# Performance work log

Measured on AMD Instinct MI355X. Metric: run time of the kernel, lower is better.

The kernel has to match this reference:

```python
import jax, jax.numpy as jnp
import numpy as np

L, D, H, N, B2 = 9, 256, 4, 1024, 4   # layers, embed dim, heads, keypoints, 2*pairs
HD = D // H
THR = 0.1
MAXM = 50


def _linear(x, W, b):
    return x @ W.T + b


def _ln(x, g, b, eps=1e-5):
    m = jnp.mean(x, -1, keepdims=True)
    v = jnp.var(x, -1, keepdims=True)
    return (x - m) * jax.lax.rsqrt(v + eps) * g + b


def _ffn(x, w1, b1, g, bb, w2, b2):
    h = _linear(x, w1, b1)
    h = jax.nn.gelu(_ln(h, g, bb), approximate=False)
    return _linear(h, w2, b2)


def _mha(q, k, v):
    b, nq, _ = q.shape
    nk = k.shape[1]
    qh = q.reshape(b, nq, H, HD)
    kh = k.reshape(b, nk, H, HD)
    vh = v.reshape(b, nk, H, HD)
    s = jnp.einsum('bqhd,bkhd->bhqk', qh, kh) * (1.0 / np.float32(np.sqrt(HD)))
    a = jax.nn.softmax(s, -1)
    return jnp.einsum('bhqk,bkhd->bqhd', a, vh).reshape(b, nq, D)


def _rotate_half(qk):  # qk: [b, n, D, 2]
    b, n, _, _ = qk.shape
    r = qk.reshape(b, n, H, HD // 2, 2, 2)
    r = jnp.stack([-r[..., 1, :], r[..., 0, :]], axis=4)
    return r.reshape(b, n, D, 2)


def _posenc(kpts, Wr):
    proj = kpts @ Wr.T                    # [b, n, HD//2]
    def expand(t):
        t = jnp.repeat(t, 2, axis=-1)     # interleave -> [b, n, HD]
        return jnp.tile(t, (1, 1, H))     # -> [b, n, D]
    return jnp.stack([expand(jnp.cos(proj)), expand(jnp.sin(proj))])  # [2, b, n, D]


def _forward(kpts, desc, posenc_Wr,
             sWqkv_w, sWqkv_b, sOut_w, sOut_b, sF1_w, sF1_b, sLN_g, sLN_b, sF2_w, sF2_b,
             cQK_w, cQK_b, cV_w, cV_b, cOut_w, cOut_b, cF1_w, cF1_b, cLN_g, cLN_b, cF2_w, cF2_b,
             fp_w, fp_b, match_w, match_b):
    enc = _posenc(kpts, posenc_Wr)
    x = desc
    idx = np.arange(B2)
    swap = idx // 2 * 2 + (1 - idx % 2)   # swap images within each pair
    for i in range(L):
        # ---- self attention with cached rotary encoding ----
        b, n, _ = x.shape
        qkv = _linear(x, sWqkv_w[i], sWqkv_b[i]).reshape(b, n, D, 3)
        qk, v = qkv[..., :2], qkv[..., 2]
        qk = enc[0][..., None] * qk + enc[1][..., None] * _rotate_half(qk)
        ctx = _mha(qk[..., 0], qk[..., 1], v)
        msg = _linear(ctx, sOut_w[i], sOut_b[i])
        x = x + _ffn(jnp.concatenate([x, msg], -1),
                     sF1_w[i], sF1_b[i], sLN_g[i], sLN_b[i], sF2_w[i], sF2_b[i])
        # ---- cross attention between images of each pair ----
        qk = _linear(x, cQK_w[i], cQK_b[i])
        v = _linear(x, cV_w[i], cV_b[i])
        m = _mha(qk, qk[swap], v[swap])
        m = _linear(m, cOut_w[i], cOut_b[i])
        x = x + _ffn(jnp.concatenate([x, m], -1),
                     cF1_w[i], cF1_b[i], cLN_g[i], cLN_b[i], cF2_w[i], cF2_b[i])
    # ---- match assignment: sigmoid log double softmax ----
    md = _linear(x, fp_w, fp_b) / (D ** 0.25)
    sim = jnp.einsum('bnd,bmd->bnm', md[0::2], md[1::2])
    z = _linear(x, match_w, match_b)      # [B2, N, 1]
    cert = jax.nn.log_sigmoid(z[0::2]) + jnp.swapaxes(jax.nn.log_sigmoid(z[1::2]), 1, 2)
    return jax.nn.log_softmax(sim, 2) + jax.nn.log_softmax(sim, 1) + cert


def _filter_matches(scores):
    B = scores.shape[0]
    m0 = jnp.argmax(scores, 2)
    m1 = jnp.argmax(scores, 1)
    mscores = jnp.exp(jnp.max(scores, 2))
    mutual = jnp.arange(N)[None, :] == jnp.take_along_axis(m1, m0, 1)
    masked = mscores * ((mscores > THR) & mutual).astype(mscores.dtype)
    topk_scores, topk_idx = jax.lax.top_k(masked, MAXM)
    topk_m1 = jnp.take_along_axis(m0, topk_idx, 1)
    b_idx = jnp.broadcast_to(jnp.arange(B)[:, None], (B, MAXM))
    matches = jnp.stack([b_idx, topk_idx, topk_m1], 2)
    return matches[0], topk_scores[0]


def setup_inputs() -> dict:
    key = jax.random.key(0)
    ks = iter(jax.random.split(key, 48))
    def w(shape, scale=0.02):
        return jax.random.normal(next(ks), shape, jnp.float32) * scale
    inp = {
        'kpts': jax.random.normal(next(ks), (B2, N, 2), jnp.float32),
        'desc': jax.random.normal(next(ks), (B2, N, D), jnp.float32),
        'posenc_Wr': w((HD // 2, 2), 1.0),  # std = gamma**-2 = 1
        'sWqkv_w': w((L, 3 * D, D)), 'sWqkv_b': w((L, 3 * D)),
        'sOut_w': w((L, D, D)), 'sOut_b': w((L, D)),
        'sF1_w': w((L, 2 * D, 2 * D)), 'sF1_b': w((L, 2 * D)),
        'sLN_g': jnp.ones((L, 2 * D), jnp.float32), 'sLN_b': jnp.zeros((L, 2 * D), jnp.float32),
        'sF2_w': w((L, D, 2 * D)), 'sF2_b': w((L, D)),
        'cQK_w': w((L, D, D)), 'cQK_b': w((L, D)),
        'cV_w': w((L, D, D)), 'cV_b': w((L, D)),
        'cOut_w': w((L, D, D)), 'cOut_b': w((L, D)),
        'cF1_w': w((L, 2 * D, 2 * D)), 'cF1_b': w((L, 2 * D)),
        'cLN_g': jnp.ones((L, 2 * D), jnp.float32), 'cLN_b': jnp.zeros((L, 2 * D), jnp.float32),
        'cF2_w': w((L, D, 2 * D)), 'cF2_b': w((L, D)),
        'fp_w': w((D, D)), 'fp_b': w((D,)),
        'match_w': w((1, D)), 'match_b': w((1,)),
    }
    return inp


def reference(kpts, desc, posenc_Wr,
              sWqkv_w, sWqkv_b, sOut_w, sOut_b, sF1_w, sF1_b, sLN_g, sLN_b, sF2_w, sF2_b,
              cQK_w, cQK_b, cV_w, cV_b, cOut_w, cOut_b, cF1_w, cF1_b, cLN_g, cLN_b, cF2_w, cF2_b,
              fp_w, fp_b, match_w, match_b):
    scores = _forward(kpts, desc, posenc_Wr,
                      sWqkv_w, sWqkv_b, sOut_w, sOut_b, sF1_w, sF1_b, sLN_g, sLN_b, sF2_w, sF2_b,
                      cQK_w, cQK_b, cV_w, cV_b, cOut_w, cOut_b, cF1_w, cF1_b, cLN_g, cLN_b, cF2_w, cF2_b,
                      fp_w, fp_b, match_w, match_b)
    matches, mscores = _filter_matches(scores)
    return scores, matches, mscores
```

## Files before the change

### kernel.cpp

```cpp
#include <hip/hip_runtime.h>
#include <hip/hip_bf16.h>
#include <math.h>

typedef __hip_bfloat16 bf16;
typedef unsigned short ushort;
typedef unsigned int u32;
typedef __attribute__((ext_vector_type(8))) short s8b;
typedef __attribute__((ext_vector_type(4))) short s4b;
typedef __attribute__((ext_vector_type(4))) float f4v;

#define Nc 1024
#define Dc 256
#define MA 4096

__device__ __forceinline__ float tofl(float v){ return v; }
__device__ __forceinline__ float tofl(bf16 v){ return __bfloat162float(v); }

__device__ __forceinline__ ushort rneu(float f){
  unsigned u = __float_as_uint(f);
  unsigned r = (u + 0x7fffu + ((u>>16)&1u)) >> 16;
  return (ushort)r;
}
__device__ __forceinline__ float ubf(ushort h){ return __uint_as_float(((unsigned)h)<<16); }

__device__ __forceinline__ float fexp2(float x){
#if __has_builtin(__builtin_amdgcn_exp2f)
  return __builtin_amdgcn_exp2f(x);
#else
  return exp2f(x);
#endif
}

__global__ void k_detect(const void* p, int* flag){
  if(threadIdx.x==0 && blockIdx.x==0){
    *flag = (((const ushort*)p)[0] == 0x3F80) ? 0 : 1;
  }
}

template<typename TIN>
__device__ void gemm_body(const float* A, const TIN* B, const TIN* bias, float* C,
                          int M, int Nout, int K, int lda, int ldb, int ldc,
                          float alpha, int accum, int dolog){
  __shared__ float As[32][33];
  __shared__ float Bs[32][33];
  int tx = threadIdx.x, ty = threadIdx.y;
  int tid = ty*16 + tx;
  int n0 = blockIdx.x*32, m0 = blockIdx.y*32;
  int lr = tid >> 3;
  int lc = (tid & 7) * 4;
  float acc00=0.f, acc01=0.f, acc10=0.f, acc11=0.f;
  for(int kk=0; kk<K; kk+=32){
    int m = m0 + lr, n = n0 + lr;
#pragma unroll
    for(int j=0;j<4;j++){
      int k = kk + lc + j;
      As[lr][lc+j] = (m < M && k < K) ? A[(size_t)m*lda + k] : 0.f;
      Bs[lr][lc+j] = (n < Nout && k < K) ? tofl(B[(size_t)n*ldb + k]) : 0.f;
    }
    __syncthreads();
#pragma unroll
    for(int k=0;k<32;k++){
      float a0 = As[ty][k],   a1 = As[ty+16][k];
      float b0 = Bs[tx][k],   b1 = Bs[tx+16][k];
      acc00 += a0*b0; acc01 += a0*b1; acc10 += a1*b0; acc11 += a1*b1;
    }
    __syncthreads();
  }
#define STORE(mm,nn,acc) do{ int m_=(mm), n_=(nn); if(m_<M && n_<Nout){ \
    float r = (acc) + (bias ? tofl(bias[n_]) : 0.f); r *= alpha; \
    if(dolog) r = fminf(r,0.f) - log1pf(expf(-fabsf(r))); \
    if(accum) C[(size_t)m_*ldc + n_] += r; else C[(size_t)m_*ldc + n_] = r; } }while(0)
  STORE(m0+ty,    n0+tx,    acc00);
  STORE(m0+ty,    n0+tx+16, acc01);
  STORE(m0+ty+16, n0+tx,    acc10);
  STORE(m0+ty+16, n0+tx+16, acc11);
#undef STORE
}

__global__ __launch_bounds__(256)
void k_gemm_w(const int* flag, const float* A, const void* Bb, long boff,
              const void* biasb, long biasoff, float* C,
              int M, int Nout, int K, int lda, int ldb, int ldc,
              float alpha, int accum, int dolog){
  if(*flag){
    const float* B = ((const float*)Bb) + boff;
    const float* bi = biasb ? ((const float*)biasb) + biasoff : nullptr;
    gemm_body<float>(A, B, bi, C, M, Nout, K, lda, ldb, ldc, alpha, accum, dolog);
  }else{
    const bf16* B = ((const bf16*)Bb) + boff;
    const bf16* bi = biasb ? ((const bf16*)biasb) + biasoff : nullptr;
    gemm_body<bf16>(A, B, bi, C, M, Nout, K, lda, ldb, ldc, alpha, accum, dolog);
  }
}

template<typename TIN>
__device__ void cast2_body(const void* in_, float* x, ushort* xh, ushort* xl, int n){
  const TIN* in = (const TIN*)in_;
  int i = blockIdx.x*256 + threadIdx.x;
  if(i >= n) return;
  float f = tofl(in[i]);
  x[i] = f;
  ushort h = rneu(f);
  xh[i] = h; xl[i] = rneu(f - ubf(h));
}
__global__ void k_cast2(const int* flag, const void* in, float* x, ushort* xh, ushort* xl, int n){
  if(*flag) cast2_body<float>(in, x, xh, xl, n); else cast2_body<bf16>(in, x, xh, xl, n);
}

template<typename TIN>
__device__ void splitw_body(const void* src_, long off, ushort* dh, ushort* dl, int n){
  const TIN* src = ((const TIN*)src_) + off;
  int i = blockIdx.x*256 + threadIdx.x;
  if(i >= n) return;
  float f = tofl(src[i]);
  ushort h = rneu(f);
  dh[i] = h; dl[i] = rneu(f - ubf(h));
}
__global__ void k_splitw(const int* flag, const void* src, long off, ushort* dh, ushort* dl, int n){
  if(*flag) splitw_body<float>(src, off, dh, dl, n); else splitw_body<bf16>(src, off, dh, dl, n);
}
template<typename TIN>
__device__ void biasf_body(const void* src_, long off, float* dst, int n){
  const TIN* src = ((const TIN*)src_) + off;
  int i = blockIdx.x*256 + threadIdx.x;
  if(i < n) dst[i] = tofl(src[i]);
}
__global__ void k_biasf(const int* flag, const void* src, long off, float* dst, int n){
  if(*flag) biasf_body<float>(src, off, dst, n); else biasf_body<bf16>(src, off, dst, n);
}

template<typename TIN>
__device__ void rotcs_body(const void* kpts_, const void* Wr_, float* cs){
  int i = blockIdx.x*256 + threadIdx.x;
  if(i >= MA*32) return;
  int m = i >> 5, p = i & 31;
  const TIN* kpts = (const TIN*)kpts_;
  const TIN* Wr   = (const TIN*)Wr_;
  float kx = tofl(kpts[m*2]), ky = tofl(kpts[m*2+1]);
  float proj = kx*tofl(Wr[p*2]) + ky*tofl(Wr[p*2+1]);
  cs[(size_t)m*64 + p*2    ] = cosf(proj);
  cs[(size_t)m*64 + p*2 + 1] = sinf(proj);
}
__global__ void k_rotcs(const int* flag, const void* kpts, const void* Wr, float* cs){
  if(*flag) rotcs_body<float>(kpts, Wr, cs); else rotcs_body<bf16>(kpts, Wr, cs);
}

template<typename TIN>
__device__ void wsl_body(int L, const void* p0,const void* p1,const void* p2,const void* p3,
                         const void* p4,const void* p5,const void* p6,const void* p7,const void* p8,
                         const void* b0,const void* b1,const void* b2,const void* b3,const void* b4,
                         const void* b5,const void* b6,const void* b7,const void* b8,
                         ushort* WH, ushort* WL, float* WB){
  int idx = blockIdx.x*256 + threadIdx.x;
  if(idx < 311296){
    int i = idx*4;
    const TIN* s;
    if(i < 196608){
      int nr = i >> 8, col = i & 255;
      int sr = (nr < 256) ? nr*3 : (nr < 512) ? (nr-256)*3+1 : (nr-512)*3+2;
      s = (const TIN*)p0 + (size_t)L*196608 + sr*256 + col;
    }
    else if(i < 262144)  s = (const TIN*)p1 + (size_t)L*65536  + (i-196608);
    else if(i < 524288)  s = (const TIN*)p2 + (size_t)L*262144 + (i-262144);
    else if(i < 655360)  s = (const TIN*)p3 + (size_t)L*131072 + (i-524288);
    else if(i < 720896)  s = (const TIN*)p4 + (size_t)L*65536  + (i-655360);
    else if(i < 786432)  s = (const TIN*)p5 + (size_t)L*65536  + (i-720896);
    else if(i < 851968)  s = (const TIN*)p6 + (size_t)L*65536  + (i-786432);
    else if(i < 1114112) s = (const TIN*)p7 + (size_t)L*262144 + (i-851968);
    else                 s = (const TIN*)p8 + (size_t)L*131072 + (i-1114112);
    float f[4];
    if constexpr(sizeof(TIN) == 4){
      f4v v = *(const f4v*)s;
      f[0]=v[0]; f[1]=v[1]; f[2]=v[2]; f[3]=v[3];
    } else {
      s4b v = *(const s4b*)s;
#pragma unroll
      for(int j=0;j<4;j++) f[j] = __uint_as_float(((u32)(ushort)v[j])<<16);
    }
    s4b hv, lv;
#pragma unroll
    for(int j=0;j<4;j++){
      ushort h = rneu(f[j]);
      hv[j] = (short)h;
      lv[j] = (short)rneu(f[j] - ubf(h));
    }
    *(s4b*)&WH[i] = hv;
    *(s4b*)&WL[i] = lv;
  } else if(idx < 311296 + 3328){
    int j = idx - 311296;
    const TIN* s;
    if(j < 768){
      int sj = (j < 256) ? j*3 : (j < 512) ? (j-256)*3+1 : (j-512)*3+2;
      s = (const TIN*)b0 + (size_t)L*768 + sj;
    }
    else if(j < 1024)  s = (const TIN*)b1 + (size_t)L*256 + (j-768);
    else if(j < 1536)  s = (const TIN*)b2 + (size_t)L*512 + (j-1024);
    else if(j < 1792)  s = (const TIN*)b3 + (size_t)L*256 + (j-1536);
    else if(j < 2048)  s = (const TIN*)b4 + (size_t)L*256 + (j-1792);
    else if(j < 2304)  s = (const TIN*)b5 + (size_t)L*256 + (j-2048);
    else if(j < 2560)  s = (const TIN*)b6 + (size_t)L*256 + (j-2304);
    else if(j < 3072)  s = (const TIN*)b7 + (size_t)L*512 + (j-2560);
    else               s = (const TIN*)b8 + (size_t)L*256 + (j-3072);
    WB[j] = tofl(*s);
  }
}
__global__ void k_wsplit(const int* flag, int L0, long strW, long strB,
    const void* p0,const void* p1,const void* p2,const void* p3,const void* p4,
    const void* p5,const void* p6,const void* p7,const void* p8,
    const void* b0,const void* b1,const void* b2,const void* b3,const void* b4,
    const void* b5,const void* b6,const void* b7,const void* b8,
    ushort* WH, ushort* WL, float* WB){
  int L = L0 + blockIdx.y;
  ushort* WHl = WH + (size_t)blockIdx.y*strW;
  ushort* WLl = WL + (size_t)blockIdx.y*strW;
  float*  WBl = WB + (size_t)blockIdx.y*strB;
  if(*flag) wsl_body<float>(L,p0,p1,p2,p3,p4,p5,p6,p7,p8,b0,b1,b2,b3,b4,b5,b6,b7,b8,WHl,WLl,WBl);
  else      wsl_body<bf16>(L,p0,p1,p2,p3,p4,p5,p6,p7,p8,b0,b1,b2,b3,b4,b5,b6,b7,b8,WHl,WLl,WBl);
}

template<int MT>
__global__ __launch_bounds__(256)
void k_gemm_mxT(const ushort* __restrict__ Ah, const ushort* __restrict__ Al,
                const ushort* __restrict__ A2h, const ushort* __restrict__ A2l, int lda,
                const ushort* __restrict__ Bh, const ushort* __restrict__ Bl, int ldb,
                const float* __restrict__ bias, float alpha,
                float* C, int ldc, int accum,
                ushort* Ch, ushort* Cl, int lds,
                ushort* keh, ushort* kel, const float* __restrict__ cs,
                ushort* vth, ushort* vtl,
                int K, int mode){
  constexpr int MFR = MT/16;
  constexpr int NACC = MFR*2;
  constexpr int MFH = MFR/2;
  __shared__ __align__(16) ushort LB[(2*MT+128)*72];
  int t = threadIdx.x;
  int n0 = blockIdx.x*64, m0 = blockIdx.y*MT;
  int w = t>>6, lane = t&63, quad = lane>>4, l15 = lane&15;
  int kg = w>>1, nh = w&1;
  int brow = t>>2, bc16 = (t&3)*16;
  int arow = (MT==64) ? (t>>2) : (t>>3);
  int acol = (MT==64) ? ((t&3)*16) : ((t&7)*8);
  f4v acc[NACC];
  f4v zz = {0.f,0.f,0.f,0.f};
#pragma unroll
  for(int j=0;j<NACC;j++) acc[j] = zz;
  int rounds = K >> 6;

  s8b r0,r1,r2,r3,r4,r5,r6,r7;
  auto gload = [&](int r){
    int k0 = r*64;
    const ushort* ah = Ah; const ushort* al = Al; int kloc = k0;
    if(A2h && k0 >= 256){ ah = A2h; al = A2l; kloc = k0 - 256; }
    const ushort* aph = &ah[(size_t)(m0+arow)*lda + kloc + acol];
    const ushort* apl = &al[(size_t)(m0+arow)*lda + kloc + acol];
    const ushort* bph = &Bh[(size_t)(n0+brow)*ldb + k0 + bc16];
    const ushort* bpl = &Bl[(size_t)(n0+brow)*ldb + k0 + bc16];
    r0 = *(const s8b*)aph;
    r2 = *(const s8b*)apl;
    if(MT==64){ r1 = *(const s8b*)(aph+8); r3 = *(const s8b*)(apl+8); }
    r4 = *(const s8b*)bph;   r5 = *(const s8b*)(bph+8);
    r6 = *(const s8b*)bpl;   r7 = *(const s8b*)(bpl+8);
  };
  auto writeS = [&](){
    *(s8b*)&LB[(arow)*72 + acol]        = r0;
    *(s8b*)&LB[(MT+arow)*72 + acol]     = r2;
    if(MT==64){
      *(s8b*)&LB[(arow)*72 + acol+8]    = r1;
      *(s8b*)&LB[(MT+arow)*72 + acol+8] = r3;
    }
    *(s8b*)&LB[(2*MT+brow)*72 + bc16]      = r4;
    *(s8b*)&LB[(2*MT+brow)*72 + bc16+8]    = r5;
    *(s8b*)&LB[(2*MT+64+brow)*72 + bc16]   = r6;
    *(s8b*)&LB[(2*MT+64+brow)*72 + bc16+8] = r7;
  };

  gload(0);
  for(int r=0; r<rounds; r++){
    __syncthreads();
    writeS();
    __syncthreads();
    s8b afh[MFR], afl[MFR], bfh[2], bfl[2];
#pragma unroll
    for(int mf=0;mf<MFR;mf++){
      afh[mf] = *(s8b*)&LB[(mf*16+l15)*72 + kg*32+quad*8];
      afl[mf] = *(s8b*)&LB[(MT+mf*16+l15)*72 + kg*32+quad*8];
    }
#pragma unroll
    for(int nf=0;nf<2;nf++){
      bfh[nf] = *(s8b*)&LB[(2*MT+nh*32+nf*16+l15)*72 + kg*32+quad*8];
      bfl[nf] = *(s8b*)&LB[(2*MT+64+nh*32+nf*16+l15)*72 + kg*32+quad*8];
    }
    if(r+1 < rounds) gload(r+1);
#pragma unroll
    for(int mf=0;mf<MFR;mf++){
#pragma unroll
      for(int nf=0;nf<2;nf++){
        int a = mf*2+nf;
        acc[a] = __builtin_amdgcn_mfma_f32_16x16x32_bf16(afh[mf], bfh[nf], acc[a], 0,0,0);
        acc[a] = __builtin_amdgcn_mfma_f32_16x16x32_bf16(afh[mf], bfl[nf], acc[a], 0,0,0);
        acc[a] = __builtin_amdgcn_mfma_f32_16x16x32_bf16(afl[mf], bfh[nf], acc[a], 0,0,0);
      }
    }
  }
  __syncthreads();
  f4v* scr = (f4v*)LB;
#pragma unroll
  for(int f=0;f<NACC;f++) scr[(w*NACC+f)*64 + lane] = acc[f];
  __syncthreads();
  int pw = w^2;
#pragma unroll
  for(int f=0;f<NACC;f++){
    f4v o = scr[(pw*NACC+f)*64 + lane];
    acc[f] += o;
  }

  bool vblk = (mode == 1 && n0 >= 512) || (mode == 3 && n0 >= 256);
  if(vblk){
    __syncthreads();
    u32* tp = (u32*)LB;
#pragma unroll
    for(int mi=0;mi<MFH;mi++){
      int mf = kg*MFH + mi;
#pragma unroll
      for(int nf=0;nf<2;nf++){
        f4v a = acc[mf*2+nf];
#pragma unroll
        for(int rr=0;rr<4;rr++){
          int ml = mf*16 + quad*4 + rr;
          int nl = nh*32 + nf*16 + l15;
          float val = a[rr];
          if(bias) val += bias[n0 + nl];
          val *= alpha;
          ushort hh = rneu(val);
          ushort ll = rneu(val - ubf(hh));
          tp[nl*(MT+1) + ml] = (u32)hh | ((u32)ll << 16);
        }
      }
    }
    __syncthreads();
    int b = m0 >> 10;
    int mloc = m0 & 1023;
    int d0 = n0 - ((mode == 1) ? 512 : 256);
    constexpr int NPASS = (MT==64) ? 2 : 1;
#pragma unroll
    for(int pass=0; pass<NPASS; pass++){
      int row, col;
      if(MT==64){ row = (t>>3) + pass*32; col = (t&7)*8; }
      else      { row = t>>2;             col = (t&3)*8; }
      int d = d0 + row;
      u32 c0=tp[row*(MT+1)+col+0], c1=tp[row*(MT+1)+col+1], c2=tp[row*(MT+1)+col+2], c3=tp[row*(MT+1)+col+3];
      u32 c4=tp[row*(MT+1)+col+4], c5=tp[row*(MT+1)+col+5], c6=tp[row*(MT+1)+col+6], c7=tp[row*(MT+1)+col+7];
      s8b hi, lo;
      hi[0]=(short)(c0&0xffff); lo[0]=(short)(c0>>16);
      hi[1]=(short)(c1&0xffff); lo[1]=(short)(c1>>16);
      hi[2]=(short)(c2&0xffff); lo[2]=(short)(c2>>16);
      hi[3]=(short)(c3&0xffff); lo[3]=(short)(c3>>16);
      hi[4]=(short)(c4&0xffff); lo[4]=(short)(c4>>16);
      hi[5]=(short)(c5&0xffff); lo[5]=(short)(c5>>16);
      hi[6]=(short)(c6&0xffff); lo[6]=(short)(c6>>16);
      hi[7]=(short)(c7&0xffff); lo[7]=(short)(c7>>16);
      size_t go = ((size_t)((b*4 + (d>>6))*64 + (d&63)))*1024 + mloc + col;
      *(s8b*)&vth[go] = hi;
      *(s8b*)&vtl[go] = lo;
    }
    return;
  }

#pragma unroll
  for(int mi=0;mi<MFH;mi++){
    int mf = kg*MFH + mi;
#pragma unroll
    for(int nf=0;nf<2;nf++){
      f4v a = acc[mf*2+nf];
#pragma unroll
      for(int rr=0;rr<4;rr++){
        int m = m0 + mf*16 + quad*4 + rr;
        int n = n0 + nh*32 + nf*16 + l15;
        float val = a[rr];
        if(bias) val += bias[n];
        val *= alpha;
        if(mode == 1){
          int d = (n < 256) ? n : (n - 256);
          const float* csp = cs + (size_t)m*64 + (d & 62);
          float cc = csp[0], ssn = csp[1];
          float pv = __shfl_xor(val, 1);
          float rv = (d & 1) ? (cc*val + ssn*pv) : (cc*val - ssn*pv);
          ushort hh = rneu(rv);
          ushort* dh = (n < 256) ? Ch : keh;
          ushort* dl = (n < 256) ? Cl : kel;
          size_t gi = (size_t)m*256 + d;
          dh[gi] = hh; dl[gi] = rneu(rv - ubf(hh));
        } else if(mode == 3){
          ushort hh = rneu(val);
          Ch[(size_t)m*256 + n] = hh;
          Cl[(size_t)m*256 + n] = rneu(val - ubf(hh));
        } else {
          if(C){
            size_t ci = (size_t)m*ldc + n;
            if(accum) val += C[ci];
            C[ci] = val;
          }
          if(Ch){
            ushort hh = rneu(val);
            Ch[(size_t)m*lds + n] = hh;
            Cl[(size_t)m*lds + n] = rneu(val - ubf(hh));
          }
        }
      }
    }
  }
}

#define FSC 0.18033688011112042f
__global__ __launch_bounds__(256)
void k_flashmx(const ushort* __restrict__ qh_, const ushort* __restrict__ ql_,
               const ushort* __restrict__ kh_, const ushort* __restrict__ kl_,
               const ushort* __restrict__ vth_, const ushort* __restrict__ vtl_,
               ushort* __restrict__ cth, ushort* __restrict__ ctl, int bxor,
               float* __restrict__ PO, float* __restrict__ PML, int nch){
  int qt = blockIdx.x, z = blockIdx.y, ch = blockIdx.z;
  int b = z>>2, h = z&3;
  int bk = b ^ bxor;
  __shared__ __align__(16) ushort Kh[64][72], Kl[64][72], Vh[64][72], Vl[64][72];
  int t = threadIdx.x, w = t>>6, lane = t&63, quad = lane>>4, l15 = lane&15;
  ushort* Psw = &Kh[w*16][0];
  s8b qfh[2], qfl[2];
  {
    size_t row = (size_t)b*1024 + qt*64 + w*16 + l15;
    const ushort* qrh = qh_ + row*256 + h*64;
    const ushort* qrl = ql_ + row*256 + h*64;
    qfh[0] = *(const s8b*)(qrh + quad*8);
    qfh[1] = *(const s8b*)(qrh + 32 + quad*8);
    qfl[0] = *(const s8b*)(qrl + quad*8);
    qfl[1] = *(const s8b*)(qrl + 32 + quad*8);
  }
  float m_i[4] = {-1e30f,-1e30f,-1e30f,-1e30f};
  float l_i[4] = {0.f,0.f,0.f,0.f};
  f4v O[4];
  f4v zz = {0.f,0.f,0.f,0.f};
#pragma unroll
  for(int dt=0;dt<4;dt++) O[dt] = zz;

  s8b rK0,rK1,rK2,rK3, rV0,rV1,rV2,rV3;
  auto stage_load = [&](int kt){
#pragma unroll
    for(int i=0;i<4;i++){
      int c = t + i*256;
      int half = c>>9, row = (c>>3)&63, o8 = (c&7)*8;
      const s8b* src = (const s8b*)((half ? kl_ : kh_) +
                       ((size_t)(bk*1024 + kt*64 + row))*256 + h*64 + o8);
      if(i==0) rK0=*src; else if(i==1) rK1=*src; else if(i==2) rK2=*src; else rK3=*src;
    }
#pragma unroll
    for(int i=0;i<4;i++){
      int c = t + i*256;
      int half = c>>9, d = (c>>3)&63, o8 = (c&7)*8;
      const s8b* src = (const s8b*)((half ? vtl_ : vth_) +
                       ((size_t)((bk*4+h)*64 + d))*1024 + kt*64 + o8);
      if(i==0) rV0=*src; else if(i==1) rV1=*src; else if(i==2) rV2=*src; else rV3=*src;
    }
  };
  auto stage_write = [&](){
#pragma unroll
    for(int i=0;i<4;i++){
      int c = t + i*256;
      int half = c>>9, row = (c>>3)&63, o8 = (c&7)*8;
      s8b v = (i==0)?rK0:(i==1)?rK1:(i==2)?rK2:rK3;
      if(half) *(s8b*)&Kl[row][o8] = v;
      else     *(s8b*)&Kh[row][o8] = v;
    }
#pragma unroll
    for(int i=0;i<4;i++){
      int c = t + i*256;
      int half = c>>9, d = (c>>3)&63, o8 = (c&7)*8;
      s8b v = (i==0)?rV0:(i==1)?rV1:(i==2)?rV2:rV3;
      if(half) *(s8b*)&Vl[d][o8] = v;
      else     *(s8b*)&Vh[d][o8] = v;
    }
  };

  int ktn = 16/nch;
  int kt0 = ch*ktn;
  stage_load(kt0);
  for(int kt=kt0; kt<kt0+ktn; kt++){
    __syncthreads();
    stage_write();
    __syncthreads();
    if(kt+1 < kt0+ktn) stage_load(kt+1);
    f4v s[4];
#pragma unroll
    for(int nt=0;nt<4;nt++) s[nt] = zz;
#pragma unroll
    for(int nt=0;nt<4;nt++){
#pragma unroll
      for(int k2=0;k2<2;k2++){
        s8b fbh = *(s8b*)&Kh[nt*16+l15][k2*32 + quad*8];
        s8b fbl = *(s8b*)&Kl[nt*16+l15][k2*32 + quad*8];
        s[nt] = __builtin_amdgcn_mfma_f32_16x16x32_bf16(qfh[k2], fbh, s[nt], 0,0,0);
        s[nt] = __builtin_amdgcn_mfma_f32_16x16x32_bf16(qfh[k2], fbl, s[nt], 0,0,0);
        s[nt] = __builtin_amdgcn_mfma_f32_16x16x32_bf16(qfl[k2], fbh, s[nt], 0,0,0);
      }
    }
    __syncthreads();
#pragma unroll
    for(int rr=0;rr<4;rr++){
      float v0=s[0][rr]*FSC, v1=s[1][rr]*FSC, v2=s[2][rr]*FSC, v3=s[3][rr]*FSC;
      float mx = fmaxf(fmaxf(v0,v1), fmaxf(v2,v3));
      mx = fmaxf(mx, __shfl_xor(mx,1));
      mx = fmaxf(mx, __shfl_xor(mx,2));
      mx = fmaxf(mx, __shfl_xor(mx,4));
      mx = fmaxf(mx, __shfl_xor(mx,8));
      float mnew = fmaxf(m_i[rr], mx);
      float al = fexp2(m_i[rr] - mnew);
      float p0 = fexp2(v0-mnew), p1 = fexp2(v1-mnew), p2 = fexp2(v2-mnew), p3 = fexp2(v3-mnew);
      float ls = p0+p1+p2+p3;
      ls += __shfl_xor(ls,1);
      ls += __shfl_xor(ls,2);
      ls += __shfl_xor(ls,4);
      ls += __shfl_xor(ls,8);
      l_i[rr] = l_i[rr]*al + ls;
      m_i[rr] = mnew;
#pragma unroll
      for(int dt=0;dt<4;dt++) O[dt][rr] *= al;
      int prow = quad*4 + rr;
      Psw[prow*72 +  0 + l15] = rneu(p0);
      Psw[prow*72 + 16 + l15] = rneu(p1);
      Psw[prow*72 + 32 + l15] = rneu(p2);
      Psw[prow*72 + 48 + l15] = rneu(p3);
    }
    s8b pf0 = *(s8b*)&Psw[l15*72 + quad*8];
    s8b pf1 = *(s8b*)&Psw[l15*72 + 32 + quad*8];
#pragma unroll
    for(int dt=0;dt<4;dt++){
#pragma unroll
      for(int k2=0;k2<2;k2++){
        s8b fvh = *(s8b*)&Vh[dt*16+l15][k2*32 + quad*8];
        s8b fvl = *(s8b*)&Vl[dt*16+l15][k2*32 + quad*8];
        s8b pf = k2 ? pf1 : pf0;
        O[dt] = __builtin_amdgcn_mfma_f32_16x16x32_bf16(pf, fvh, O[dt], 0,0,0);
        O[dt] = __builtin_amdgcn_mfma_f32_16x16x32_bf16(pf, fvl, O[dt], 0,0,0);
      }
    }
  }
  if(nch == 1){
#pragma unroll
    for(int rr=0;rr<4;rr++){
      float inv = 1.f / l_i[rr];
      int row = qt*64 + w*16 + quad*4 + rr;
#pragma unroll
      for(int dt=0;dt<4;dt++){
        float val = O[dt][rr]*inv;
        size_t gi = ((size_t)b*1024 + row)*256 + h*64 + dt*16 + l15;
        ushort hh = rneu(val);
        cth[gi] = hh; ctl[gi] = rneu(val - ubf(hh));
      }
    }
  } else {
    size_t tb = (size_t)(z*16+qt)*nch + ch;
    float* po  = PO  + tb*4096;
    float* pml = PML + tb*128;
#pragma unroll
    for(int rr=0;rr<4;rr++){
      int row = w*16 + quad*4 + rr;
#pragma unroll
      for(int dt=0;dt<4;dt++){
        po[row*64 + dt*16 + l15] = O[dt][rr];
      }
      if(l15 == 0){
        pml[row]      = m_i[rr];
        pml[64 + row] = l_i[rr];
      }
    }
  }
}

__global__ __launch_bounds__(256)
void k_fmerge(const float* __restrict__ PO, const float* __restrict__ PML,
              ushort* __restrict__ cth, ushort* __restrict__ ctl){
  int qt = blockIdx.x, z = blockIdx.y;
  int b = z>>2, h = z&3;
  int t = threadIdx.x;
  int row = t>>2, dg = (t&3)*16;
  size_t tb0 = (size_t)(z*16+qt)*4;
  float m0 = PML[(tb0+0)*128 + row], m1 = PML[(tb0+1)*128 + row];
  float m2 = PML[(tb0+2)*128 + row], m3 = PML[(tb0+3)*128 + row];
  float M = fmaxf(fmaxf(m0,m1), fmaxf(m2,m3));
  float w0 = fexp2(m0-M), w1 = fexp2(m1-M), w2 = fexp2(m2-M), w3 = fexp2(m3-M);
  float L = PML[(tb0+0)*128 + 64 + row]*w0 + PML[(tb0+1)*128 + 64 + row]*w1
          + PML[(tb0+2)*128 + 64 + row]*w2 + PML[(tb0+3)*128 + 64 + row]*w3;
  float inv = 1.f/L;
  const f4v* p0 = (const f4v*)(PO + (tb0+0)*4096 + row*64 + dg);
  const f4v* p1 = (const f4v*)(PO + (tb0+1)*4096 + row*64 + dg);
  const f4v* p2 = (const f4v*)(PO + (tb0+2)*4096 + row*64 + dg);
  const f4v* p3 = (const f4v*)(PO + (tb0+3)*4096 + row*64 + dg);
  size_t gi = ((size_t)b*1024 + qt*64 + row)*256 + h*64 + dg;
#pragma unroll
  for(int j=0;j<4;j++){
    f4v o = p0[j]*w0 + p1[j]*w1 + p2[j]*w2 + p3[j]*w3;
#pragma unroll
    for(int e=0;e<4;e++){
      float val = o[e]*inv;
      ushort hh = rneu(val);
      cth[gi + j*4 + e] = hh;
      ctl[gi + j*4 + e] = rneu(val - ubf(hh));
    }
  }
}

template<typename TIN>
__device__ void ln2_body(const float* h, ushort* hh, ushort* hl, const TIN* g, const TIN* bb){
  __shared__ float ws8[8];
  int r = blockIdx.x; int t = threadIdx.x;
  int w = t>>6, lane = t&63;
  const float* row = h + (size_t)r*512;
  float a = row[t], b_ = row[t+256];
  float s = a + b_;
#pragma unroll
  for(int off=1; off<64; off<<=1) s += __shfl_xor(s, off);
  if(lane==0) ws8[w] = s;
  __syncthreads();
  float mean = (ws8[0]+ws8[1]+ws8[2]+ws8[3])*(1.f/512.f);
  float da = a-mean, db = b_-mean;
  float v = da*da + db*db;
#pragma unroll
  for(int off=1; off<64; off<<=1) v += __shfl_xor(v, off);
  if(lane==0) ws8[4+w] = v;
  __syncthreads();
  float rstd = rsqrtf((ws8[4]+ws8[5]+ws8[6]+ws8[7])*(1.f/512.f) + 1e-5f);
  float na = da*rstd*tofl(g[t])     + tofl(bb[t]);
  float nb = db*rstd*tofl(g[t+256]) + tofl(bb[t+256]);
  float ga = 0.5f*na*(1.f + erff(na*0.70710678f));
  float gb = 0.5f*nb*(1.f + erff(nb*0.70710678f));
  size_t base = (size_t)r*512;
  ushort u0 = rneu(ga); hh[base+t] = u0; hl[base+t] = rneu(ga - ubf(u0));
  ushort u1 = rneu(gb); hh[base+t+256] = u1; hl[base+t+256] = rneu(gb - ubf(u1));
}
__global__ void k_ln_gelu2(const int* flag, const float* h, ushort* hh, ushort* hl,
                           const void* gb, long goff, const void* bbb, long boff){
  if(*flag) ln2_body<float>(h, hh, hl, ((const float*)gb)+goff, ((const float*)bbb)+boff);
  else      ln2_body<bf16>(h, hh, hl, ((const bf16*)gb)+goff, ((const bf16*)bbb)+boff);
}

__global__ void k_lse_rows(const float* __restrict__ sim, float* __restrict__ rlse){
  const float* row = sim + (size_t)blockIdx.x*Nc;
  __shared__ float red[256];
  int t = threadIdx.x;
  float v0=row[t],v1=row[t+256],v2=row[t+512],v3=row[t+768];
  float mx = fmaxf(fmaxf(v0,v1),fmaxf(v2,v3));
  red[t]=mx; __syncthreads();
  for(int s=128;s>0;s>>=1){ if(t<s) red[t]=fmaxf(red[t],red[t+s]); __syncthreads(); }
  mx = red[0]; __syncthreads();
  red[t]=expf(v0-mx)+expf(v1-mx)+expf(v2-mx)+expf(v3-mx); __syncthreads();
  for(int s=128;s>0;s>>=1){ if(t<s) red[t]+=red[t+s]; __syncthreads(); }
  if(t==0) rlse[blockIdx.x] = mx + logf(red[0]);
}

__global__ void k_lse_cols2(const float* __restrict__ sim, float* __restrict__ clse){
  __shared__ float Rm[16][16], Rs[16][16];
  int t = threadIdx.x;
  int c = t & 15, s = t >> 4;
  int col = blockIdx.x*16 + c;
  const float* base = sim + col;
  float mx = -1e30f, sum = 0.f;
  for(int n=s*64; n<s*64+64; n++){
    float v = base[(size_t)n*1024];
    if(v > mx){ sum = sum*expf(mx - v) + 1.f; mx = v; }
    else sum += expf(v - mx);
  }
  Rm[s][c] = mx; Rs[s][c] = sum; __syncthreads();
  for(int off=8; off>0; off>>=1){
    if(s < off){
      float m2 = Rm[s+off][c], s2 = Rs[s+off][c];
      float m1 = Rm[s][c], s1 = Rs[s][c];
      float m = fmaxf(m1, m2);
      Rm[s][c] = m;
      Rs[s][c] = s1*expf(m1-m) + s2*expf(m2-m);
    }
    __syncthreads();
  }
  if(s == 0) clse[col] = Rm[0][c] + logf(Rs[0][c]);
}

__global__ __launch_bounds__(256)
void k_final2r(float* __restrict__ out, const float* __restrict__ rlse,
               const float* __restrict__ clse, const float* __restrict__ lsg,
               int* __restrict__ m0, float* __restrict__ msc){
  int blk = blockIdx.x;
  int p = blk >> 10, n = blk & 1023;
  int t = threadIdx.x;
  int w = t>>6, lane = t&63;
  size_t base = (size_t)blk*1024;
  float rl = rlse[blk];
  float lgn = lsg[p*2048 + n];
  const float* lgm = lsg + p*2048 + 1024;
  const float* cl = clse + p*1024;
  float bv = -1e30f; int bi = 0;
#pragma unroll
  for(int j=0;j<4;j++){
    int m = t + j*256;
    float v = 2.f*out[base+m] - rl - cl[m] + lgn + lgm[m];
    out[base+m] = v;
    if(v > bv){ bv = v; bi = m; }
  }
  if(p) return;
#pragma unroll
  for(int off=1; off<64; off<<=1){
    float v2 = __shfl_xor(bv, off); int i2 = __shfl_xor(bi, off);
    if(v2 > bv || (v2 == bv && i2 < bi)){ bv = v2; bi = i2; }
  }
  __shared__ float wv[4]; __shared__ int wi[4];
  if(lane==0){ wv[w]=bv; wi[w]=bi; }
  __syncthreads();
  if(t==0){
#pragma unroll
    for(int k=1;k<4;k++){
      if(wv[k] > wv[0] || (wv[k]==wv[0] && wi[k] < wi[0])){ wv[0]=wv[k]; wi[0]=wi[k]; }
    }
    m0[n] = wi[0]; msc[n] = expf(wv[0]);
  }
}

__global__ void k_amax_cols2(const float* __restrict__ sc, int* __restrict__ m1){
  __shared__ float Rv[16][16]; __shared__ int Ri[16][16];
  int t = threadIdx.x;
  int c = t & 15, s = t >> 4;
  int col = blockIdx.x*16 + c;
  float bv = -1e30f; int bi = 0;
  for(int n=s*64; n<s*64+64; n++){
    float v = sc[(size_t)n*1024 + col];
    if(v > bv){ bv = v; bi = n; }
  }
  Rv[s][c]=bv; Ri[s][c]=bi; __syncthreads();
  for(int off=8; off>0; off>>=1){
    if(s < off){
      if(Rv[s+off][c] > Rv[s][c]){ Rv[s][c]=Rv[s+off][c]; Ri[s][c]=Ri[s+off][c]; }
    }
    __syncthreads();
  }
  if(s == 0) m1[col] = Ri[0][c];
}

__global__ __launch_bounds__(128)
void k_topk(const int* __restrict__ m0, const int* __restrict__ m1,
            const float* __restrict__ msc, float* __restrict__ out){
  __shared__ float V[1024];
  int t = threadIdx.x;
  for(int i2=t; i2<1024; i2+=128){
    float mv = msc[i2];
    V[i2] = (mv > 0.1f && m1[m0[i2]] == i2) ? mv : 0.f;
  }
  __syncthreads();
  int i = blockIdx.x*128 + t;
  float vi = V[i];
  int r = 0;
#pragma unroll 8
  for(int j=0;j<1024;j++){
    float vj = V[j];
    r += (vj > vi || (vj == vi && j < i)) ? 1 : 0;
  }
  if(r < 50){
    out[2*Nc*Nc + r*3 + 0] = 0.f;
    out[2*Nc*Nc + r*3 + 1] = (float)i;
    out[2*Nc*Nc + r*3 + 2] = (float)m0[i];
    out[2*Nc*Nc + 150 + r] = vi;
  }
}

extern "C" void kernel_launch(void* const* d_in, const int* in_sizes, int n_in,
                              void* d_out, int out_size, void* d_ws, size_t ws_size,
                              hipStream_t stream){
  const void* kpts    = d_in[0];
  const void* desc    = d_in[1];
  const void* Wr      = d_in[2];
  const void* sWqkv_w = d_in[3];
  const void* sWqkv_b = d_in[4];
  const void* sOut_w  = d_in[5];
  const void* sOut_b  = d_in[6];
  const void* sF1_w   = d_in[7];
  const void* sF1_b   = d_in[8];
  const void* sLN_g   = d_in[9];
  const void* sLN_b   = d_in[10];
  const void* sF2_w   = d_in[11];
  const void* sF2_b   = d_in[12];
  const void* cQK_w   = d_in[13];
  const void* cQK_b   = d_in[14];
  const void* cV_w    = d_in[15];
  const void* cV_b    = d_in[16];
  const void* cOut_w  = d_in[17];
  const void* cOut_b  = d_in[18];
  const void* cF1_w   = d_in[19];
  const void* cF1_b   = d_in[20];
  const void* cLN_g   = d_in[21];
  const void* cLN_b   = d_in[22];
  const void* cF2_w   = d_in[23];
  const void* cF2_b   = d_in[24];
  const void* fp_w    = d_in[25];
  const void* fp_b    = d_in[26];
  const void* match_w = d_in[27];
  const void* match_b = d_in[28];

  float* ws  = (float*)d_ws;
  float* out = (float*)d_out;
  int* flag = (int*)d_ws;
  float* zbuf = ws + 64;
  float* rlse = ws + 4160;
  float* clse = ws + 6208;
  float* msc  = ws + 12352;
  int*   m0i  = (int*)(ws + 13376);
  int*   m1i  = (int*)(ws + 14400);

  bool presplit = ws_size >= (size_t)20759552*4 + 1024;
  size_t wW = presplit ? 5603328 : 622592;
  size_t wB = presplit ? 32768   : 4096;

  size_t o = 16384;
  ushort* WH = (ushort*)(ws + o); o += wW;
  ushort* WL = (ushort*)(ws + o); o += wW;
  float*  WB = ws + o;            o += wB;
  ushort* fpWH = (ushort*)(ws + o); o += 32768;
  ushort* fpWL = (ushort*)(ws + o); o += 32768;
  float*  fpB  = ws + o;            o += 1024;
  float*  x  = ws + o;              o += 1048576;
  ushort* xh = (ushort*)(ws + o);   o += 524288;
  ushort* xl = (ushort*)(ws + o);   o += 524288;
  float*  hbuf = ws + o;            o += 2097152;
  ushort* qsh = (ushort*)(ws + o);  o += 524288;
  ushort* qsl = (ushort*)(ws + o);  o += 524288;
  ushort* ksh = (ushort*)(ws + o);  o += 524288;
  ushort* ksl = (ushort*)(ws + o);  o += 524288;
  ushort* vth = (ushort*)(ws + o);  o += 524288;
  ushort* vtl = (ushort*)(ws + o);  o += 524288;
  ushort* cth = (ushort*)(ws + o);  o += 524288;
  ushort* ctl = (ushort*)(ws + o);  o += 524288;
  ushort* mgh = (ushort*)(ws + o);  o += 524288;
  ushort* mgl = (ushort*)(ws + o);  o += 524288;
  ushort* hsh = qsh;
  ushort* hsl = ksh;
  ushort* mdh = cth;
  ushort* mdl = ctl;

  float* cs = out;

  float* PO  = ws + o;
  float* PML = ws + o + 4194304;
  int nch = (ws_size >= (size_t)(20759552 + 4194304 + 131072)*4 + 1024) ? 4 : 1;

  auto MX = [&](const ushort* Ah, const ushort* Al, const ushort* A2h, const ushort* A2l,
                int lda, const ushort* Bh, const ushort* Bl, int ldb,
                const float* bias, float alpha, float* C, int ldc, int accum,
                ushort* Ch, ushort* Cl, int lds,
                ushort* keh, ushort* kel, ushort* vh, ushort* vl,
                int M, int Nout, int K, int mode, int mt){
    dim3 g(Nout/64, M/mt);
    if(mt == 32)
      k_gemm_mxT<32><<<g, 256, 0, stream>>>(Ah,Al,A2h,A2l,lda,Bh,Bl,ldb,bias,alpha,C,ldc,accum,
                                            Ch,Cl,lds,keh,kel,cs,vh,vl,K,mode);
    else
      k_gemm_mxT<64><<<g, 256, 0, stream>>>(Ah,Al,A2h,A2l,lda,Bh,Bl,ldb,bias,alpha,C,ldc,accum,
                                            Ch,Cl,lds,keh,kel,cs,vh,vl,K,mode);
  };
  auto FLASH = [&](const ushort* qh, const ushort* ql, const ushort* kh, const ushort* kl,
                   int bxor){
    k_flashmx<<<dim3(16,16,nch), 256, 0, stream>>>(qh,ql,kh,kl,vth,vtl, cth,ctl, bxor,
                                                   PO, PML, nch);
    if(nch == 4) k_fmerge<<<dim3(16,16), 256, 0, stream>>>(PO, PML, cth, ctl);
  };

  k_detect<<<1, 64, 0, stream>>>(sLN_g, flag);
  k_splitw<<<(65536+255)/256, 256, 0, stream>>>(flag, fp_w, 0, fpWH, fpWL, 65536);
  k_biasf<<<1, 256, 0, stream>>>(flag, fp_b, 0, fpB, 256);
  k_cast2<<<(MA*Dc+255)/256, 256, 0, stream>>>(flag, desc, x, xh, xl, MA*Dc);
  k_rotcs<<<(MA*32+255)/256, 256, 0, stream>>>(flag, kpts, Wr, cs);

  if(presplit){
    dim3 g((311296+3328+255)/256, 9);
    k_wsplit<<<g, 256, 0, stream>>>(flag, 0, 1245184, 3328,
      sWqkv_w, sOut_w, sF1_w, sF2_w, cQK_w, cV_w, cOut_w, cF1_w, cF2_w,
      sWqkv_b, sOut_b, sF1_b, sF2_b, cQK_b, cV_b, cOut_b, cF1_b, cF2_b,
      WH, WL, WB);
  }

  for(int i=0;i<9;i++){
    if(!presplit){
      dim3 g((311296+3328+255)/256, 1);
      k_wsplit<<<g, 256, 0, stream>>>(flag, i, 0, 0,
        sWqkv_w, sOut_w, sF1_w, sF2_w, cQK_w, cV_w, cOut_w, cF1_w, cF2_w,
        sWqkv_b, sOut_b, sF1_b, sF2_b, cQK_b, cV_b, cOut_b, cF1_b, cF2_b,
        WH, WL, WB);
    }
    const ushort* WHl = presplit ? WH + (size_t)i*1245184 : WH;
    const ushort* WLl = presplit ? WL + (size_t)i*1245184 : WL;
    const float*  WBl = presplit ? WB + (size_t)i*3328    : WB;

    MX(xh,xl,nullptr,nullptr,256, WHl+0,WLl+0,256, WBl+0, 1.f,
       nullptr,0,0, qsh,qsl,0, ksh,ksl, vth,vtl, MA,768,256, 1, 32);
    FLASH(qsh,qsl,ksh,ksl, 0);
    MX(cth,ctl,nullptr,nullptr,256, WHl+196608,WLl+196608,256, WBl+768, 1.f,
       nullptr,0,0, mgh,mgl,256, nullptr,nullptr, nullptr,nullptr, MA,256,256, 0, 32);
    MX(xh,xl,mgh,mgl,256, WHl+262144,WLl+262144,512, WBl+1024, 1.f,
       hbuf,512,0, nullptr,nullptr,0, nullptr,nullptr, nullptr,nullptr, MA,512,512, 0, 32);
    k_ln_gelu2<<<MA, 256, 0, stream>>>(flag, hbuf, hsh, hsl, sLN_g, (long)i*512, sLN_b, (long)i*512);
    MX(hsh,hsl,nullptr,nullptr,512, WHl+524288,WLl+524288,512, WBl+1536, 1.f,
       x,256,1, xh,xl,256, nullptr,nullptr, nullptr,nullptr, MA,256,512, 0, 32);
    MX(xh,xl,nullptr,nullptr,256, WHl+655360,WLl+655360,256, WBl+1792, 1.f,
       nullptr,0,0, qsh,qsl,0, nullptr,nullptr, vth,vtl, MA,512,256, 3, 32);
    FLASH(qsh,qsl,qsh,qsl, 1);
    MX(cth,ctl,nullptr,nullptr,256, WHl+786432,WLl+786432,256, WBl+2304, 1.f,
       nullptr,0,0, mgh,mgl,256, nullptr,nullptr, nullptr,nullptr, MA,256,256, 0, 32);
    MX(xh,xl,mgh,mgl,256, WHl+851968,WLl+851968,512, WBl+2560, 1.f,
       hbuf,512,0, nullptr,nullptr,0, nullptr,nullptr, nullptr,nullptr, MA,512,512, 0, 32);
    k_ln_gelu2<<<MA, 256, 0, stream>>>(flag, hbuf, hsh, hsl, cLN_g, (long)i*512, cLN_b, (long)i*512);
    MX(hsh,hsl,nullptr,nullptr,512, WHl+1114112,WLl+1114112,512, WBl+3072, 1.f,
       x,256,1, xh,xl,256, nullptr,nullptr, nullptr,nullptr, MA,256,512, 0, 32);
  }

  MX(xh,xl,nullptr,nullptr,256, fpWH,fpWL,256, fpB, 0.25f,
     nullptr,0,0, mdh,mdl,256, nullptr,nullptr, nullptr,nullptr, MA,256,256, 0, 32);
  k_gemm_w<<<dim3(1,128), dim3(16,16), 0, stream>>>(flag, x, match_w, 0, match_b, 0,
                                                    zbuf, MA, 1, 256, 256, 256, 1, 1.f, 0, 1);
  MX(mdh,mdl,nullptr,nullptr,256, mdh + (size_t)1024*256, mdl + (size_t)1024*256, 256,
     nullptr, 1.f, out,1024,0, nullptr,nullptr,0, nullptr,nullptr, nullptr,nullptr, 1024,1024,256, 0, 32);
  MX(mdh + (size_t)2048*256, mdl + (size_t)2048*256,nullptr,nullptr,256,
     mdh + (size_t)3072*256, mdl + (size_t)3072*256, 256,
     nullptr, 1.f, out+1048576,1024,0, nullptr,nullptr,0, nullptr,nullptr, nullptr,nullptr, 1024,1024,256, 0, 32);

  k_lse_rows<<<2048, 256, 0, stream>>>(out, rlse);
  k_lse_cols2<<<64, 256, 0, stream>>>(out, clse);
  k_lse_cols2<<<64, 256, 0, stream>>>(out + 1048576, clse + 1024);
  k_final2r<<<2048, 256, 0, stream>>>(out, rlse, clse, zbuf, m0i, msc);
  k_amax_cols2<<<64, 256, 0, stream>>>(out, m1i);
  k_topk<<<8, 128, 0, stream>>>(m0i, m1i, msc, out);
}
```

Before: 1.988 ms.

## Fold attention output projection into first FFN weight half

Adds a kernel that precomputes W1b·Wout and the matching bias term, so the FFN's first GEMM reads the attention context directly. This removes the separate output-projection GEMM in both the self and cross blocks of every layer, along with its message buffer round trip. In exchange it adds a weight-combination pass per layer and changes rounding, because the fused weights are stored again as a bf16 hi/lo pair.

```diff
diff --git a/kernel.cpp b/kernel.cpp
--- a/kernel.cpp
+++ b/kernel.cpp
@@ -216,6 +216,47 @@
   float*  WBl = WB + (size_t)blockIdx.y*strB;
   if(*flag) wsl_body<float>(L,p0,p1,p2,p3,p4,p5,p6,p7,p8,b0,b1,b2,b3,b4,b5,b6,b7,b8,WHl,WLl,WBl);
   else      wsl_body<bf16>(L,p0,p1,p2,p3,p4,p5,p6,p7,p8,b0,b1,b2,b3,b4,b5,b6,b7,b8,WHl,WLl,WBl);
+}
+
+__global__ __launch_bounds__(256)
+void k_wcomb(ushort* WH, ushort* WL, float* WB, long strW, long strB){
+  __shared__ float w1b[32][256];
+  int strip = blockIdx.x;
+  int c = blockIdx.y;
+  int L = c >> 1, br = c & 1;
+  size_t wbase = (size_t)L*strW + (br ? 851968 : 262144);
+  size_t obase = (size_t)L*strW + (br ? 786432 : 196608);
+  float* WBl  = WB + (size_t)L*strB;
+  float* b1   = WBl + (br ? 2560 : 1024);
+  float* bout = WBl + (br ? 2304 : 768);
+  int t = threadIdx.x;
+  int o0 = strip*32;
+  for(int idx = t; idx < 32*256; idx += 256){
+    int o = idx >> 8, j = idx & 255;
+    size_t s = wbase + (size_t)(o0+o)*512 + 256 + j;
+    w1b[o][j] = ubf(WH[s]) + ubf(WL[s]);
+  }
+  __syncthreads();
+  float acc[32];
+#pragma unroll
+  for(int o=0;o<32;o++) acc[o] = 0.f;
+  for(int j=0;j<256;j++){
+    size_t s = obase + (size_t)j*256 + t;
+    float wv = ubf(WH[s]) + ubf(WL[s]);
+#pragma unroll
+    for(int o=0;o<32;o++) acc[o] += w1b[o][j]*wv;
+  }
+#pragma unroll
+  for(int o=0;o<32;o++){
+    size_t s = wbase + (size_t)(o0+o)*512 + 256 + t;
+    ushort hh = rneu(acc[o]);
+    WH[s] = hh; WL[s] = rneu(acc[o] - ubf(hh));
+  }
+  if(t < 32){
+    float s = 0.f;
+    for(int j=0;j<256;j++) s += w1b[t][j]*bout[j];
+    b1[o0 + t] += s;
+  }
 }
 
 template<int MT>
@@ -878,6 +919,7 @@
       sWqkv_w, sOut_w, sF1_w, sF2_w, cQK_w, cV_w, cOut_w, cF1_w, cF2_w,
       sWqkv_b, sOut_b, sF1_b, sF2_b, cQK_b, cV_b, cOut_b, cF1_b, cF2_b,
       WH, WL, WB);
+    k_wcomb<<<dim3(16, 18), 256, 0, stream>>>(WH, WL, WB, 1245184, 3328);
   }
 
   for(int i=0;i<9;i++){
@@ -887,6 +929,7 @@
         sWqkv_w, sOut_w, sF1_w, sF2_w, cQK_w, cV_w, cOut_w, cF1_w, cF2_w,
         sWqkv_b, sOut_b, sF1_b, sF2_b, cQK_b, cV_b, cOut_b, cF1_b, cF2_b,
         WH, WL, WB);
+      k_wcomb<<<dim3(16, 2), 256, 0, stream>>>(WH, WL, WB, 0, 0);
     }
     const ushort* WHl = presplit ? WH + (size_t)i*1245184 : WH;
     const ushort* WLl = presplit ? WL + (size_t)i*1245184 : WL;
@@ -895,9 +938,7 @@
     MX(xh,xl,nullptr,nullptr,256, WHl+0,WLl+0,256, WBl+0, 1.f,
        nullptr,0,0, qsh,qsl,0, ksh,ksl, vth,vtl, MA,768,256, 1, 32);
     FLASH(qsh,qsl,ksh,ksl, 0);
-    MX(cth,ctl,nullptr,nullptr,256, WHl+196608,WLl+196608,256, WBl+768, 1.f,
-       nullptr,0,0, mgh,mgl,256, nullptr,nullptr, nullptr,nullptr, MA,256,256, 0, 32);
-    MX(xh,xl,mgh,mgl,256, WHl+262144,WLl+262144,512, WBl+1024, 1.f,
+    MX(xh,xl,cth,ctl,256, WHl+262144,WLl+262144,512, WBl+1024, 1.f,
        hbuf,512,0, nullptr,nullptr,0, nullptr,nullptr, nullptr,nullptr, MA,512,512, 0, 32);
     k_ln_gelu2<<<MA, 256, 0, stream>>>(flag, hbuf, hsh, hsl, sLN_g, (long)i*512, sLN_b, (long)i*512);
     MX(hsh,hsl,nullptr,nullptr,512, WHl+524288,WLl+524288,512, WBl+1536, 1.f,
@@ -905,9 +946,7 @@
     MX(xh,xl,nullptr,nullptr,256, WHl+655360,WLl+655360,256, WBl+1792, 1.f,
        nullptr,0,0, qsh,qsl,0, nullptr,nullptr, vth,vtl, MA,512,256, 3, 32);
     FLASH(qsh,qsl,qsh,qsl, 1);
-    MX(cth,ctl,nullptr,nullptr,256, WHl+786432,WLl+786432,256, WBl+2304, 1.f,
-       nullptr,0,0, mgh,mgl,256, nullptr,nullptr, nullptr,nullptr, MA,256,256, 0, 32);
-    MX(xh,xl,mgh,mgl,256, WHl+851968,WLl+851968,512, WBl+2560, 1.f,
+    MX(xh,xl,cth,ctl,256, WHl+851968,WLl+851968,512, WBl+2560, 1.f,
        hbuf,512,0, nullptr,nullptr,0, nullptr,nullptr, nullptr,nullptr, MA,512,512, 0, 32);
     k_ln_gelu2<<<MA, 256, 0, stream>>>(flag, hbuf, hsh, hsl, cLN_g, (long)i*512, cLN_b, (long)i*512);
     MX(hsh,hsl,nullptr,nullptr,512, WHl+1114112,WLl+1114112,512, WBl+3072, 1.f,
```

Result: faster. 1.937 ms (-2.6%).
